# Performance work log

Hardware: AMD Instinct MI355X
Metric: run time of the kernel (lower is better)

## Reference

```python
import jax, jax.numpy as jnp
import numpy as np

B, D, H, O, E = 1048576, 17, 8, 6, 4  # batch, input_dim, expert_hidden, output_dim, n_clusters
G1, G2 = 64, 32  # gating hidden dims


def setup_inputs() -> dict:
    key = jax.random.key(0)
    ks = jax.random.split(key, 14)
    def w(k, shape, fan_in):
        return (jax.random.normal(k, shape, jnp.float32) / jnp.sqrt(jnp.float32(fan_in)))
    return {
        "x": jax.random.normal(ks[0], (B, D), jnp.float32),
        # per-expert MLP params, stacked on leading expert axis E
        "eW1": w(ks[1], (E, D, H), D), "eb1": w(ks[2], (E, H), D),
        "eW2": w(ks[3], (E, H, H), H), "eb2": w(ks[4], (E, H), H),
        "eW3": w(ks[5], (E, H, O), H), "eb3": w(ks[6], (E, O), H),
        # gating classifier params
        "gW1": w(ks[7], (D, G1), D), "gb1": w(ks[8], (G1,), D),
        "gW2": w(ks[9], (G1, G2), G1), "gb2": w(ks[10], (G2,), G1),
        "gW3": w(ks[11], (G2, E), G2), "gb3": w(ks[12], (E,), G2),
    }


def reference(x, eW1, eb1, eW2, eb2, eW3, eb3, gW1, gb1, gW2, gb2, gW3, gb3):
    # gating network: 17 -> 64 -> 32 -> 4 logits
    h = jax.nn.relu(x @ gW1 + gb1)
    h = jax.nn.relu(h @ gW2 + gb2)
    gating_logits = h @ gW3 + gb3  # [B, E]
    selected = jnp.argmax(gating_logits, axis=1)  # [B] hard routing
    # all experts computed (as in the original), stacked over expert axis
    e = jax.nn.relu(jnp.einsum('bi,eih->beh', x, eW1) + eb1)   # [B, E, H]
    e = jax.nn.relu(jnp.einsum('beh,ehk->bek', e, eW2) + eb2)  # [B, E, H]
    eo = jnp.einsum('bek,eko->beo', e, eW3) + eb3              # [B, E, O]
    # gather the selected expert's output per sample
    predictions = jnp.take_along_axis(eo, selected[:, None, None], axis=1)[:, 0, :]  # [B, O]
    return predictions, gating_logits
```

## Files before the change

### kernel.cpp

```cpp
#include <hip/hip_runtime.h>

#define BTOT 1048576
#define D 17
#define H 8
#define OUT 6
#define E 4
#define G1 64
#define G2 32

typedef short bf8 __attribute__((ext_vector_type(8)));
typedef float f4 __attribute__((ext_vector_type(4), aligned(16)));
typedef float f4u __attribute__((ext_vector_type(4), aligned(4)));
typedef float f2u __attribute__((ext_vector_type(2), aligned(4)));
typedef unsigned int u4 __attribute__((ext_vector_type(4)));

#define MFMA16 __builtin_amdgcn_mfma_f32_16x16x32_bf16

__device__ __forceinline__ unsigned int fbits(float x){ union{float f; unsigned int u;} a; a.f = x; return a.u; }
__device__ __forceinline__ float bitsf(unsigned int u){ union{unsigned int u; float f;} a; a.u = u; return a.f; }
__device__ __forceinline__ unsigned short bf_rne(float x){ unsigned int u = fbits(x); u += 0x7FFFu + ((u>>16)&1u); return (unsigned short)(u>>16); }

__device__ __forceinline__ void split2(float a, float b,
                                       unsigned int& q1, unsigned int& q2, unsigned int& q3){
    unsigned int ua = fbits(a), ub = fbits(b);
    unsigned int a1 = ua & 0xFFFF0000u, b1 = ub & 0xFFFF0000u;
    float ra = a - bitsf(a1), rb = b - bitsf(b1);
    unsigned int a2 = fbits(ra) & 0xFFFF0000u, b2 = fbits(rb) & 0xFFFF0000u;
    float ra2 = ra - bitsf(a2), rb2 = rb - bitsf(b2);
    unsigned int a3 = fbits(ra2); a3 += 0x7FFFu + ((a3>>16)&1u);
    unsigned int b3 = fbits(rb2); b3 += 0x7FFFu + ((b3>>16)&1u);
    q1 = b1 | (a1 >> 16);
    q2 = b2 | (a2 >> 16);
    q3 = (b3 & 0xFFFF0000u) | (a3 >> 16);
}

__device__ __forceinline__ void split8(f4 lo, f4 hi, bf8& A1, bf8& A2, bf8& A3){
    unsigned int p1[4], p2[4], p3[4];
    split2(lo.x, lo.y, p1[0], p2[0], p3[0]);
    split2(lo.z, lo.w, p1[1], p2[1], p3[1]);
    split2(hi.x, hi.y, p1[2], p2[2], p3[2]);
    split2(hi.z, hi.w, p1[3], p2[3], p3[3]);
    union { u4 u; bf8 s; } r1, r2, r3;
    r1.u = (u4){p1[0], p1[1], p1[2], p1[3]};
    r2.u = (u4){p2[0], p2[1], p2[2], p2[3]};
    r3.u = (u4){p3[0], p3[1], p3[2], p3[3]};
    A1 = r1.s; A2 = r2.s; A3 = r3.s;
}

__device__ __forceinline__ unsigned short split_level(float w, int l){
    unsigned int u1 = fbits(w) & 0xFFFF0000u;
    if (l == 0) return (unsigned short)(u1 >> 16);
    float r = w - bitsf(u1);
    unsigned int u2 = fbits(r) & 0xFFFF0000u;
    if (l == 1) return (unsigned short)(u2 >> 16);
    float r2 = r - bitsf(u2);
    return bf_rne(r2);
}

__global__ void hybrid_pre(const float* __restrict__ eW1, const float* __restrict__ eW2,
                           const float* __restrict__ eW3, const float* __restrict__ gW1,
                           const float* __restrict__ gW2, unsigned short* __restrict__ wsB)
{
    const int t = threadIdx.x;
    for (int i = t; i < 3*64*32; i += 256) {
        int k = i & 31, n = (i >> 5) & 63, l = i >> 11;
        float w = (k < D) ? gW1[k*G1 + n] : 0.f;
        wsB[i] = split_level(w, l);
    }
    for (int i = t; i < 3*32*64; i += 256) {
        int k = i & 63, n = (i >> 6) & 31, l = i >> 11;
        float w = gW2[k*G2 + n];
        wsB[6144 + i] = split_level(w, l);
    }
    for (int i = t; i < 1024; i += 256) {
        int k = i & 31, n = i >> 5, e = n >> 3, h = n & 7;
        float w = (k < D) ? eW1[(e*D + k)*H + h] : 0.f;
        wsB[12288 + i] = bf_rne(w);
    }
    for (int i = t; i < 1024; i += 256) {
        int k = i & 31, n = i >> 5, e = n >> 3, j = n & 7, kk = k - e*8;
        float w = (kk >= 0 && kk < 8) ? eW2[(e*H + kk)*H + j] : 0.f;
        wsB[13312 + i] = bf_rne(w);
    }
    for (int i = t; i < 512; i += 256) {
        int k = i & 31, n = i >> 5, e = k >> 3, kk = k & 7;
        float w = (n < OUT) ? eW3[(e*H + kk)*OUT + n] : 0.f;
        wsB[14336 + i] = bf_rne(w);
    }
}

__global__ __launch_bounds__(256, 2) void hybrid_main(
    const float* __restrict__ x,
    const float* __restrict__ eb1, const float* __restrict__ eb2, const float* __restrict__ eb3,
    const float* __restrict__ gb1, const float* __restrict__ gb2,
    const float* __restrict__ gW3, const float* __restrict__ gb3,
    const unsigned short* __restrict__ wsB,
    float* __restrict__ out)
{
    __shared__ char lds_all[4 * 16384];
    const int tid = threadIdx.x;
    const int wave = tid >> 6, lane = tid & 63;
    const int q = lane >> 4, c = lane & 15;
    char* slice = lds_all + wave * 16384;
    float* sx   = (float*)slice;
    float* sh1  = (float*)slice;
    float* sh2  = (float*)slice;
    unsigned short* sAe2 = (unsigned short*)slice;
    unsigned short* sAe3 = (unsigned short*)(slice + 5120);
    float* spred = (float*)(slice + 10240);
    int*   ssel  = (int*)(slice + 12288);

    const long long samp0 = (long long)blockIdx.x * 256 + wave * 64;

    {
        const float* xr = x + (samp0 + lane) * D;
        f4u x0 = *(const f4u*)xr, x1 = *(const f4u*)(xr+4);
        f4u x2 = *(const f4u*)(xr+8), x3 = *(const f4u*)(xr+12);
        float x16 = xr[16];
        float* dst = sx + lane * 36;
        *(f4*)(dst)      = (f4){x0.x,x0.y,x0.z,x0.w};
        *(f4*)(dst + 4)  = (f4){x1.x,x1.y,x1.z,x1.w};
        *(f4*)(dst + 8)  = (f4){x2.x,x2.y,x2.z,x2.w};
        *(f4*)(dst + 12) = (f4){x3.x,x3.y,x3.z,x3.w};
        *(f4*)(dst + 16) = (f4){x16, 0.f, 0.f, 0.f};
        *(f4*)(dst + 20) = (f4){0.f,0.f,0.f,0.f};
        *(f4*)(dst + 24) = (f4){0.f,0.f,0.f,0.f};
        *(f4*)(dst + 28) = (f4){0.f,0.f,0.f,0.f};
    }
    __builtin_amdgcn_wave_barrier();

    bf8 B1f[4][3];
    #pragma unroll
    for (int nt = 0; nt < 4; ++nt)
        #pragma unroll
        for (int l = 0; l < 3; ++l)
            B1f[nt][l] = *(const bf8*)(wsB + ((l*64 + nt*16 + c)*32 + q*8));
    float bias1[4];
    #pragma unroll
    for (int nt = 0; nt < 4; ++nt) bias1[nt] = gb1[nt*16 + c];

    bf8 A1[4], A2[4], A3[4];
    #pragma unroll
    for (int mt = 0; mt < 4; ++mt) {
        const float* src = sx + (mt*16 + c)*36 + q*8;
        f4 lo = *(const f4*)src, hi = *(const f4*)(src + 4);
        split8(lo, hi, A1[mt], A2[mt], A3[mt]);
    }
    __builtin_amdgcn_wave_barrier();

    #pragma unroll
    for (int mt = 0; mt < 4; ++mt) {
        #pragma unroll
        for (int nt = 0; nt < 4; ++nt) {
            f4 am = {0.f,0.f,0.f,0.f}, ac = {0.f,0.f,0.f,0.f};
            am = MFMA16(A1[mt], B1f[nt][0], am, 0,0,0);
            ac = MFMA16(A1[mt], B1f[nt][1], ac, 0,0,0);
            ac = MFMA16(A2[mt], B1f[nt][0], ac, 0,0,0);
            ac = MFMA16(A1[mt], B1f[nt][2], ac, 0,0,0);
            ac = MFMA16(A2[mt], B1f[nt][1], ac, 0,0,0);
            ac = MFMA16(A3[mt], B1f[nt][0], ac, 0,0,0);
            ac = MFMA16(A3[mt], B1f[nt][1], ac, 0,0,0);
            #pragma unroll
            for (int r = 0; r < 4; ++r) {
                float h = fmaxf(am[r] + ac[r] + bias1[nt], 0.f);
                int row = mt*16 + q*4 + r;
                int blk = (nt*2 + (c>>3)) ^ (row & 7);
                sh1[row*64 + blk*8 + (c&7)] = h;
            }
        }
    }
    __builtin_amdgcn_wave_barrier();

    bf8 B2f[2][2][3];
    #pragma unroll
    for (int nt = 0; nt < 2; ++nt)
        #pragma unroll
        for (int ks = 0; ks < 2; ++ks)
            #pragma unroll
            for (int l = 0; l < 3; ++l)
                B2f[nt][ks][l] = *(const bf8*)(wsB + 6144 + ((l*32 + nt*16 + c)*64 + ks*32 + q*8));
    float bias2[2];
    #pragma unroll
    for (int nt = 0; nt < 2; ++nt) bias2[nt] = gb2[nt*16 + c];

    #pragma unroll
    for (int mt = 0; mt < 4; ++mt) {
        bf8 C1[2], C2[2], C3[2];
        #pragma unroll
        for (int ks = 0; ks < 2; ++ks) {
            int row = mt*16 + c;
            int blk = (ks*4 + q) ^ (row & 7);
            const float* src = sh1 + row*64 + blk*8;
            f4 lo = *(const f4*)src, hi = *(const f4*)(src + 4);
            split8(lo, hi, C1[ks], C2[ks], C3[ks]);
        }
        #pragma unroll
        for (int nt = 0; nt < 2; ++nt) {
            f4 am = {0.f,0.f,0.f,0.f}, ac = {0.f,0.f,0.f,0.f};
            #pragma unroll
            for (int ks = 0; ks < 2; ++ks) {
                am = MFMA16(C1[ks], B2f[nt][ks][0], am, 0,0,0);
                ac = MFMA16(C1[ks], B2f[nt][ks][1], ac, 0,0,0);
                ac = MFMA16(C2[ks], B2f[nt][ks][0], ac, 0,0,0);
                ac = MFMA16(C1[ks], B2f[nt][ks][2], ac, 0,0,0);
                ac = MFMA16(C2[ks], B2f[nt][ks][1], ac, 0,0,0);
                ac = MFMA16(C3[ks], B2f[nt][ks][0], ac, 0,0,0);
                ac = MFMA16(C3[ks], B2f[nt][ks][1], ac, 0,0,0);
            }
            #pragma unroll
            for (int r = 0; r < 4; ++r) {
                float h = fmaxf(am[r] + ac[r] + bias2[nt], 0.f);
                int row = mt*16 + q*4 + r;
                sh2[row*36 + nt*16 + c] = h;
            }
        }
    }
    __builtin_amdgcn_wave_barrier();

    {
        const float* hr = sh2 + lane*36;
        f4 hv[8];
        #pragma unroll
        for (int i = 0; i < 8; ++i) hv[i] = *(const f4*)(hr + i*4);
        float lg[E];
        #pragma unroll
        for (int e = 0; e < E; ++e) lg[e] = gb3[e];
        #pragma unroll
        for (int k = 0; k < G2; ++k) {
            float h = hv[k>>2][k&3];
            #pragma unroll
            for (int e = 0; e < E; ++e)
                lg[e] = __builtin_fmaf(h, gW3[k*E + e], lg[e]);
        }
        int sel = 0; float best = lg[0];
        #pragma unroll
        for (int e = 1; e < E; ++e) if (lg[e] > best) { best = lg[e]; sel = e; }
        ssel[lane] = sel;
        float* lo = out + (long long)BTOT * OUT + (samp0 + lane) * E;
        *(f4*)lo = (f4){lg[0], lg[1], lg[2], lg[3]};
    }
    __builtin_amdgcn_wave_barrier();

    bf8 Be1f[2], Be2f[2], Be3f;
    #pragma unroll
    for (int nt = 0; nt < 2; ++nt) {
        Be1f[nt] = *(const bf8*)(wsB + 12288 + (nt*16 + c)*32 + q*8);
        Be2f[nt] = *(const bf8*)(wsB + 13312 + (nt*16 + c)*32 + q*8);
    }
    Be3f = *(const bf8*)(wsB + 14336 + c*32 + q*8);
    float be1v[2], be2v[2];
    #pragma unroll
    for (int nt = 0; nt < 2; ++nt) { be1v[nt] = eb1[nt*16 + c]; be2v[nt] = eb2[nt*16 + c]; }

    #pragma unroll
    for (int mt = 0; mt < 4; ++mt) {
        #pragma unroll
        for (int nt = 0; nt < 2; ++nt) {
            f4 acc = {0.f,0.f,0.f,0.f};
            acc = MFMA16(A1[mt], Be1f[nt], acc, 0,0,0);
            #pragma unroll
            for (int r = 0; r < 4; ++r) {
                float t = fmaxf(acc[r] + be1v[nt], 0.f);
                int row = mt*16 + q*4 + r;
                sAe2[row*40 + nt*16 + c] = (unsigned short)(fbits(t) >> 16);
            }
        }
    }
    __builtin_amdgcn_wave_barrier();

    #pragma unroll
    for (int mt = 0; mt < 4; ++mt) {
        bf8 Af = *(const bf8*)(sAe2 + (mt*16 + c)*40 + q*8);
        f4 acc[2];
        #pragma unroll
        for (int nt = 0; nt < 2; ++nt) {
            acc[nt] = (f4){0.f,0.f,0.f,0.f};
            acc[nt] = MFMA16(Af, Be2f[nt], acc[nt], 0,0,0);
        }
        #pragma unroll
        for (int r = 0; r < 4; ++r) {
            int row = mt*16 + q*4 + r;
            int se = ssel[row];
            #pragma unroll
            for (int nt = 0; nt < 2; ++nt) {
                int ecol = nt*2 + (c>>3);
                float t = (se == ecol) ? fmaxf(acc[nt][r] + be2v[nt], 0.f) : 0.f;
                sAe3[row*40 + nt*16 + c] = (unsigned short)(fbits(t) >> 16);
            }
        }
    }
    __builtin_amdgcn_wave_barrier();

    #pragma unroll
    for (int mt = 0; mt < 4; ++mt) {
        bf8 Af = *(const bf8*)(sAe3 + (mt*16 + c)*40 + q*8);
        f4 acc = {0.f,0.f,0.f,0.f};
        acc = MFMA16(Af, Be3f, acc, 0,0,0);
        #pragma unroll
        for (int r = 0; r < 4; ++r) {
            int row = mt*16 + q*4 + r;
            int se = ssel[row];
            if (c < OUT) spred[row*8 + c] = acc[r] + eb3[se*OUT + c];
        }
    }
    __builtin_amdgcn_wave_barrier();

    {
        const float* pr = spred + lane*8;
        f4 p0 = *(const f4*)pr;
        float p4 = pr[4], p5 = pr[5];
        float* po = out + (samp0 + lane) * OUT;
        *(f4u*)po = p0;
        *(f2u*)(po + 4) = (f2u){p4, p5};
    }
}

extern "C" void kernel_launch(void* const* d_in, const int* in_sizes, int n_in,
                              void* d_out, int out_size, void* d_ws, size_t ws_size,
                              hipStream_t stream) {
    const float* x   = (const float*)d_in[0];
    const float* eW1 = (const float*)d_in[1];
    const float* eb1 = (const float*)d_in[2];
    const float* eW2 = (const float*)d_in[3];
    const float* eb2 = (const float*)d_in[4];
    const float* eW3 = (const float*)d_in[5];
    const float* eb3 = (const float*)d_in[6];
    const float* gW1 = (const float*)d_in[7];
    const float* gb1 = (const float*)d_in[8];
    const float* gW2 = (const float*)d_in[9];
    const float* gb2 = (const float*)d_in[10];
    const float* gW3 = (const float*)d_in[11];
    const float* gb3 = (const float*)d_in[12];
    float* out = (float*)d_out;
    unsigned short* wsB = (unsigned short*)d_ws;

    hipLaunchKernelGGL(hybrid_pre, dim3(1), dim3(256), 0, stream,
                       eW1, eW2, eW3, gW1, gW2, wsB);
    hipLaunchKernelGGL(hybrid_main, dim3(BTOT / 256), dim3(256), 0, stream,
                       x, eb1, eb2, eb3, gb1, gb2, gW3, gb3, wsB, out);
}
```

Measured before the change: 220.2 us.

## Fuse gating layers per row tile and shrink LDS to raise occupancy

Loads x directly from global memory into MFMA A fragments instead of staging it through LDS. Layers 1 and 2 of the gating MLP are fused per 16-row tile, using a small padded transposed buffer (stride 67) in place of the full 64x64 swizzled h1 buffer. This shrinks per-wave LDS from 16KB to 13KB and raises the launch bounds to 3 blocks per CU, aiming for higher occupancy and less LDS traffic. The costs are scalar LDS reads on odd strides, uncoalesced row-wise global loads of x, and more register pressure from hoisting the B2 fragments.

```diff
diff --git a/kernel.cpp b/kernel.cpp
--- a/kernel.cpp
+++ b/kernel.cpp
@@ -89,7 +89,7 @@
     }
 }
 
-__global__ __launch_bounds__(256, 2) void hybrid_main(
+__global__ __launch_bounds__(256, 3) void hybrid_main(
     const float* __restrict__ x,
     const float* __restrict__ eb1, const float* __restrict__ eb2, const float* __restrict__ eb3,
     const float* __restrict__ gb1, const float* __restrict__ gb2,
@@ -97,37 +97,19 @@
     const unsigned short* __restrict__ wsB,
     float* __restrict__ out)
 {
-    __shared__ char lds_all[4 * 16384];
+    __shared__ char lds_all[4 * 13312];
     const int tid = threadIdx.x;
     const int wave = tid >> 6, lane = tid & 63;
     const int q = lane >> 4, c = lane & 15;
-    char* slice = lds_all + wave * 16384;
-    float* sx   = (float*)slice;
-    float* sh1  = (float*)slice;
-    float* sh2  = (float*)slice;
+    char* slice = lds_all + wave * 13312;
+    float* sh1t = (float*)slice;
+    float* sh2  = (float*)(slice + 4352);
+    int*   ssel = (int*)(slice + 12800);
     unsigned short* sAe2 = (unsigned short*)slice;
     unsigned short* sAe3 = (unsigned short*)(slice + 5120);
     float* spred = (float*)(slice + 10240);
-    int*   ssel  = (int*)(slice + 12288);
 
     const long long samp0 = (long long)blockIdx.x * 256 + wave * 64;
-
-    {
-        const float* xr = x + (samp0 + lane) * D;
-        f4u x0 = *(const f4u*)xr, x1 = *(const f4u*)(xr+4);
-        f4u x2 = *(const f4u*)(xr+8), x3 = *(const f4u*)(xr+12);
-        float x16 = xr[16];
-        float* dst = sx + lane * 36;
-        *(f4*)(dst)      = (f4){x0.x,x0.y,x0.z,x0.w};
-        *(f4*)(dst + 4)  = (f4){x1.x,x1.y,x1.z,x1.w};
-        *(f4*)(dst + 8)  = (f4){x2.x,x2.y,x2.z,x2.w};
-        *(f4*)(dst + 12) = (f4){x3.x,x3.y,x3.z,x3.w};
-        *(f4*)(dst + 16) = (f4){x16, 0.f, 0.f, 0.f};
-        *(f4*)(dst + 20) = (f4){0.f,0.f,0.f,0.f};
-        *(f4*)(dst + 24) = (f4){0.f,0.f,0.f,0.f};
-        *(f4*)(dst + 28) = (f4){0.f,0.f,0.f,0.f};
-    }
-    __builtin_amdgcn_wave_barrier();
 
     bf8 B1f[4][3];
     #pragma unroll
@@ -135,99 +117,91 @@
         #pragma unroll
         for (int l = 0; l < 3; ++l)
             B1f[nt][l] = *(const bf8*)(wsB + ((l*64 + nt*16 + c)*32 + q*8));
-    float bias1[4];
+    bf8 B2f[2][2][3];
+    #pragma unroll
+    for (int nt = 0; nt < 2; ++nt)
+        #pragma unroll
+        for (int ks = 0; ks < 2; ++ks)
+            #pragma unroll
+            for (int l = 0; l < 3; ++l)
+                B2f[nt][ks][l] = *(const bf8*)(wsB + 6144 + ((l*32 + nt*16 + c)*64 + ks*32 + q*8));
+    float bias1[4], bias2[2];
     #pragma unroll
     for (int nt = 0; nt < 4; ++nt) bias1[nt] = gb1[nt*16 + c];
-
-    bf8 A1[4], A2[4], A3[4];
+    #pragma unroll
+    for (int nt = 0; nt < 2; ++nt) bias2[nt] = gb2[nt*16 + c];
+
+    bf8 A1[4];
+
     #pragma unroll
     for (int mt = 0; mt < 4; ++mt) {
-        const float* src = sx + (mt*16 + c)*36 + q*8;
-        f4 lo = *(const f4*)src, hi = *(const f4*)(src + 4);
-        split8(lo, hi, A1[mt], A2[mt], A3[mt]);
-    }
-    __builtin_amdgcn_wave_barrier();
-
-    #pragma unroll
-    for (int mt = 0; mt < 4; ++mt) {
+        const float* rp = x + (samp0 + mt*16 + c) * D;
+        f4 lo = {0.f,0.f,0.f,0.f}, hi = {0.f,0.f,0.f,0.f};
+        if (q < 2) {
+            f4u a = *(const f4u*)(rp + q*8), b = *(const f4u*)(rp + q*8 + 4);
+            lo = (f4){a.x,a.y,a.z,a.w}; hi = (f4){b.x,b.y,b.z,b.w};
+        } else if (q == 2) {
+            lo.x = rp[16];
+        }
+        bf8 A2, A3;
+        split8(lo, hi, A1[mt], A2, A3);
+
         #pragma unroll
         for (int nt = 0; nt < 4; ++nt) {
             f4 am = {0.f,0.f,0.f,0.f}, ac = {0.f,0.f,0.f,0.f};
             am = MFMA16(A1[mt], B1f[nt][0], am, 0,0,0);
             ac = MFMA16(A1[mt], B1f[nt][1], ac, 0,0,0);
-            ac = MFMA16(A2[mt], B1f[nt][0], ac, 0,0,0);
+            ac = MFMA16(A2,     B1f[nt][0], ac, 0,0,0);
             ac = MFMA16(A1[mt], B1f[nt][2], ac, 0,0,0);
-            ac = MFMA16(A2[mt], B1f[nt][1], ac, 0,0,0);
-            ac = MFMA16(A3[mt], B1f[nt][0], ac, 0,0,0);
-            ac = MFMA16(A3[mt], B1f[nt][1], ac, 0,0,0);
+            ac = MFMA16(A2,     B1f[nt][1], ac, 0,0,0);
+            ac = MFMA16(A3,     B1f[nt][0], ac, 0,0,0);
+            ac = MFMA16(A3,     B1f[nt][1], ac, 0,0,0);
             #pragma unroll
             for (int r = 0; r < 4; ++r) {
                 float h = fmaxf(am[r] + ac[r] + bias1[nt], 0.f);
-                int row = mt*16 + q*4 + r;
-                int blk = (nt*2 + (c>>3)) ^ (row & 7);
-                sh1[row*64 + blk*8 + (c&7)] = h;
-            }
-        }
-    }
-    __builtin_amdgcn_wave_barrier();
-
-    bf8 B2f[2][2][3];
-    #pragma unroll
-    for (int nt = 0; nt < 2; ++nt)
-        #pragma unroll
-        for (int ks = 0; ks < 2; ++ks)
-            #pragma unroll
-            for (int l = 0; l < 3; ++l)
-                B2f[nt][ks][l] = *(const bf8*)(wsB + 6144 + ((l*32 + nt*16 + c)*64 + ks*32 + q*8));
-    float bias2[2];
-    #pragma unroll
-    for (int nt = 0; nt < 2; ++nt) bias2[nt] = gb2[nt*16 + c];
-
-    #pragma unroll
-    for (int mt = 0; mt < 4; ++mt) {
-        bf8 C1[2], C2[2], C3[2];
+                sh1t[(q*4 + r)*67 + nt*16 + c] = h;
+            }
+        }
+        __builtin_amdgcn_wave_barrier();
+
+        f4 am2[2], ac2[2];
+        am2[0] = am2[1] = ac2[0] = ac2[1] = (f4){0.f,0.f,0.f,0.f};
         #pragma unroll
         for (int ks = 0; ks < 2; ++ks) {
-            int row = mt*16 + c;
-            int blk = (ks*4 + q) ^ (row & 7);
-            const float* src = sh1 + row*64 + blk*8;
-            f4 lo = *(const f4*)src, hi = *(const f4*)(src + 4);
-            split8(lo, hi, C1[ks], C2[ks], C3[ks]);
-        }
-        #pragma unroll
-        for (int nt = 0; nt < 2; ++nt) {
-            f4 am = {0.f,0.f,0.f,0.f}, ac = {0.f,0.f,0.f,0.f};
-            #pragma unroll
-            for (int ks = 0; ks < 2; ++ks) {
-                am = MFMA16(C1[ks], B2f[nt][ks][0], am, 0,0,0);
-                ac = MFMA16(C1[ks], B2f[nt][ks][1], ac, 0,0,0);
-                ac = MFMA16(C2[ks], B2f[nt][ks][0], ac, 0,0,0);
-                ac = MFMA16(C1[ks], B2f[nt][ks][2], ac, 0,0,0);
-                ac = MFMA16(C2[ks], B2f[nt][ks][1], ac, 0,0,0);
-                ac = MFMA16(C3[ks], B2f[nt][ks][0], ac, 0,0,0);
-                ac = MFMA16(C3[ks], B2f[nt][ks][1], ac, 0,0,0);
-            }
+            const float* src = sh1t + c*67 + ks*32 + q*8;
+            f4 lo2 = {src[0], src[1], src[2], src[3]};
+            f4 hi2 = {src[4], src[5], src[6], src[7]};
+            bf8 C1, C2, C3;
+            split8(lo2, hi2, C1, C2, C3);
+            #pragma unroll
+            for (int nt = 0; nt < 2; ++nt) {
+                am2[nt] = MFMA16(C1, B2f[nt][ks][0], am2[nt], 0,0,0);
+                ac2[nt] = MFMA16(C1, B2f[nt][ks][1], ac2[nt], 0,0,0);
+                ac2[nt] = MFMA16(C2, B2f[nt][ks][0], ac2[nt], 0,0,0);
+                ac2[nt] = MFMA16(C1, B2f[nt][ks][2], ac2[nt], 0,0,0);
+                ac2[nt] = MFMA16(C2, B2f[nt][ks][1], ac2[nt], 0,0,0);
+                ac2[nt] = MFMA16(C3, B2f[nt][ks][0], ac2[nt], 0,0,0);
+                ac2[nt] = MFMA16(C3, B2f[nt][ks][1], ac2[nt], 0,0,0);
+            }
+        }
+        #pragma unroll
+        for (int nt = 0; nt < 2; ++nt)
             #pragma unroll
             for (int r = 0; r < 4; ++r) {
-                float h = fmaxf(am[r] + ac[r] + bias2[nt], 0.f);
-                int row = mt*16 + q*4 + r;
-                sh2[row*36 + nt*16 + c] = h;
-            }
-        }
-    }
-    __builtin_amdgcn_wave_barrier();
+                float h = fmaxf(am2[nt][r] + ac2[nt][r] + bias2[nt], 0.f);
+                sh2[(mt*16 + q*4 + r)*33 + nt*16 + c] = h;
+            }
+        __builtin_amdgcn_wave_barrier();
+    }
 
     {
-        const float* hr = sh2 + lane*36;
-        f4 hv[8];
-        #pragma unroll
-        for (int i = 0; i < 8; ++i) hv[i] = *(const f4*)(hr + i*4);
+        const float* hr = sh2 + lane*33;
         float lg[E];
         #pragma unroll
         for (int e = 0; e < E; ++e) lg[e] = gb3[e];
         #pragma unroll
         for (int k = 0; k < G2; ++k) {
-            float h = hv[k>>2][k&3];
+            float h = hr[k];
             #pragma unroll
             for (int e = 0; e < E; ++e)
                 lg[e] = __builtin_fmaf(h, gW3[k*E + e], lg[e]);
@@ -261,8 +235,7 @@
             #pragma unroll
             for (int r = 0; r < 4; ++r) {
                 float t = fmaxf(acc[r] + be1v[nt], 0.f);
-                int row = mt*16 + q*4 + r;
-                sAe2[row*40 + nt*16 + c] = (unsigned short)(fbits(t) >> 16);
+                sAe2[(mt*16 + q*4 + r)*40 + nt*16 + c] = (unsigned short)(fbits(t) >> 16);
             }
         }
     }
```

New measurement: 224.4 us. No clear change (+1.9%).
